# Optimization experiments

Measured on AMD Instinct MI355X. Metric: run time of the kernel, lower is better.

## Reference

```python
import jax, jax.numpy as jnp
import numpy as np

N_HEADS = 16
N_KV_HEADS = 4
HEAD_DIM = 128
D_MODEL = 2048
WINDOW = 1024
THETA = 10000.0
EPS = 1e-6


def _rmsnorm(x, w):
    var = jnp.mean(x * x, axis=-1, keepdims=True)
    return x * jax.lax.rsqrt(var + EPS) * w


def _rope(x, pos):
    # x: [B, H, S, D]; rotate-half (llama-style) RoPE
    d2 = HEAD_DIM // 2
    inv_freq = 1.0 / (THETA ** (jnp.arange(0, HEAD_DIM, 2, dtype=jnp.float32) / HEAD_DIM))
    ang = pos[:, None].astype(jnp.float32) * inv_freq[None, :]  # [S, D/2]
    cos = jnp.cos(ang)[None, None]
    sin = jnp.sin(ang)[None, None]
    x1, x2 = x[..., :d2], x[..., d2:]
    return jnp.concatenate([x1 * cos - x2 * sin, x1 * sin + x2 * cos], axis=-1)


def setup_inputs() -> dict:
    key = jax.random.key(0)
    ks = jax.random.split(key, 7)
    B, S = 1, 2048
    s = 0.02
    return {
        "x": jax.random.normal(ks[0], (B, S, D_MODEL), jnp.float32),
        "wq": jax.random.normal(ks[1], (N_HEADS * HEAD_DIM, D_MODEL), jnp.float32) * s,
        "wk": jax.random.normal(ks[2], (N_KV_HEADS * HEAD_DIM, D_MODEL), jnp.float32) * s,
        "wv": jax.random.normal(ks[3], (N_KV_HEADS * HEAD_DIM, D_MODEL), jnp.float32) * s,
        "wo": jax.random.normal(ks[4], (D_MODEL, N_HEADS * HEAD_DIM), jnp.float32) * s,
        "q_norm_w": jnp.ones((HEAD_DIM,), jnp.float32),
        "k_norm_w": jnp.ones((HEAD_DIM,), jnp.float32),
    }


def reference(x, wq, wk, wv, wo, q_norm_w, k_norm_w):
    B, S, _ = x.shape
    past_length = 0
    scale = HEAD_DIM ** -0.5
    n_rep = N_HEADS // N_KV_HEADS

    q = (x @ wq.T).reshape(B, S, N_HEADS, HEAD_DIM).transpose(0, 2, 1, 3)
    k = (x @ wk.T).reshape(B, S, N_KV_HEADS, HEAD_DIM).transpose(0, 2, 1, 3)
    v = (x @ wv.T).reshape(B, S, N_KV_HEADS, HEAD_DIM).transpose(0, 2, 1, 3)

    q = _rmsnorm(q, q_norm_w)
    k = _rmsnorm(k, k_norm_w)

    pos = jnp.arange(S) + past_length
    q = _rope(q, pos)
    k = _rope(k, pos)

    # GQA: materialize repeated KV heads, as in _repeat_kv
    k_rep = jnp.repeat(k, n_rep, axis=1)  # [B, H, S, D]
    v_rep = jnp.repeat(v, n_rep, axis=1)

    # sliding-window causal mask (total_seq_len=S > WINDOW)
    q_idx = jnp.arange(S)[:, None] + past_length
    k_idx = jnp.arange(S)[None, :]
    mask = (q_idx >= k_idx) & (q_idx - k_idx < WINDOW)  # [S, S]

    scores = jnp.einsum("bhqd,bhkd->bhqk", q, k_rep) * scale
    scores = jnp.where(mask[None, None], scores, jnp.float32(-jnp.inf))
    attn = jax.nn.softmax(scores, axis=-1)
    out = jnp.einsum("bhqk,bhkd->bhqd", attn, v_rep)

    out = out.transpose(0, 2, 1, 3).reshape(B, S, N_HEADS * HEAD_DIM)
    return out @ wo.T
```

## Files before the change

kernel.cpp:

```cpp
#include <hip/hip_runtime.h>
#include <hip/hip_bf16.h>
#include <cstdint>
#include <cstddef>

typedef __attribute__((ext_vector_type(4))) float f32x4;
typedef __attribute__((ext_vector_type(8))) short bf16x8;
typedef __attribute__((ext_vector_type(8))) unsigned short us8;

#define MFMA16(a, b, c) __builtin_amdgcn_mfma_f32_16x16x32_bf16(a, b, c, 0, 0, 0)

__device__ inline unsigned short f2bf(float f) {
    unsigned int u = __float_as_uint(f);
    u += 0x7fffu + ((u >> 16) & 1u);
    return (unsigned short)(u >> 16);
}
__device__ inline float bf2f(unsigned short u) {
    return __uint_as_float((unsigned int)u << 16);
}
__device__ inline unsigned short f2bf_fast(float f) {
    float r;
    asm("v_cvt_pk_bf16_f32 %0, %1, %2" : "=v"(r) : "v"(f), "v"(f));
    return (unsigned short)__float_as_uint(r);
}

__device__ inline void gload_lds16(const void* g, void* l) {
    __builtin_amdgcn_global_load_lds(
        (const __attribute__((address_space(1))) void*)g,
        (__attribute__((address_space(3))) void*)l, 16, 0, 0);
}
__device__ inline unsigned lds_addr(const void* p) {
    return (unsigned)(size_t)((__attribute__((address_space(3))) const void*)p);
}

__global__ __launch_bounds__(256) void prep_all(const float* __restrict__ x,
                                                const float* __restrict__ wq,
                                                const float* __restrict__ wk,
                                                const float* __restrict__ wv,
                                                const float* __restrict__ wo,
                                                unsigned short* __restrict__ xb,
                                                unsigned short* __restrict__ wqkv,
                                                unsigned short* __restrict__ wob,
                                                float2* __restrict__ tbl) {
    const int b = blockIdx.x;
    if (b < 14336) {
        const float* src; unsigned short* dst; int off4;
        if (b < 4096)       { src = x;  dst = xb;                 off4 = b; }
        else if (b < 8192)  { src = wq; dst = wqkv;               off4 = b - 4096; }
        else if (b < 9216)  { src = wk; dst = wqkv + 2048 * 2048; off4 = b - 8192; }
        else if (b < 10240) { src = wv; dst = wqkv + 2560 * 2048; off4 = b - 9216; }
        else                { src = wo; dst = wob;                off4 = b - 10240; }
        int i = (off4 * 256 + threadIdx.x) * 4;
        float4 v = *(const float4*)(src + i);
        ushort4 o;
        o.x = f2bf(v.x); o.y = f2bf(v.y); o.z = f2bf(v.z); o.w = f2bf(v.w);
        *(ushort4*)(dst + i) = o;
    } else {
        int idx = (b - 14336) * 256 + threadIdx.x;
        int row = idx >> 6, t = idx & 63;
        float inv_freq = exp2f((float)t * (-2.0f / 128.0f) * 13.287712379549449f);
        float s, c;
        sincosf((float)row * inv_freq, &s, &c);
        tbl[idx] = make_float2(c, s);
    }
}

__global__ __launch_bounds__(512, 2) void gemm256(const unsigned short* __restrict__ A,
                                                  const unsigned short* __restrict__ B,
                                                  unsigned short* __restrict__ Cp,
                                                  int M, int N, int Kfull, int kspan) {
    __shared__ unsigned short As[3][8192];
    __shared__ unsigned short Bs[3][8192];
    const int tid = threadIdx.x;
    const int lane = tid & 63, wave = tid >> 6;
    const int wr = wave >> 2, wc = wave & 3;
    const int l15 = lane & 15, l4 = lane >> 4;
    const int gx = gridDim.x;
    const int nwg = gx * gridDim.y;
    const int bid0 = blockIdx.y * gx + blockIdx.x;
    const int q8 = nwg >> 3, r8 = nwg & 7;
    const int xcd = bid0 & 7, sub = bid0 >> 3;
    const int wgid = ((xcd < r8) ? xcd * (q8 + 1) : r8 * (q8 + 1) + (xcd - r8) * q8) + sub;
    const int bm = wgid / gx, bn = wgid % gx;
    const int z = blockIdx.z;
    const unsigned short* Az = A + (size_t)z * kspan;
    const unsigned short* Bz = B + (size_t)z * kspan;
    unsigned short* C = Cp + (size_t)z * M * N;
    const int nK = kspan >> 5;

    f32x4 acc[8][4] = {};

    const int r0 = tid >> 2, qs = tid & 3;
    const int qsw = qs ^ ((r0 >> 1) & 3);
    const unsigned short* pa0 = Az + (size_t)(bm * 256 + r0) * Kfull + qsw * 8;
    const unsigned short* pa1 = pa0 + (size_t)128 * Kfull;
    const unsigned short* pb0 = Bz + (size_t)(bn * 256 + r0) * Kfull + qsw * 8;
    const unsigned short* pb1 = pb0 + (size_t)128 * Kfull;

#define STG(kt, bb)                                            \
    do {                                                       \
        gload_lds16(pa0 + (kt) * 32, &As[bb][tid * 8]);        \
        gload_lds16(pa1 + (kt) * 32, &As[bb][4096 + tid * 8]); \
        gload_lds16(pb0 + (kt) * 32, &Bs[bb][tid * 8]);        \
        gload_lds16(pb1 + (kt) * 32, &Bs[bb][4096 + tid * 8]); \
    } while (0)

    const int q = l4 ^ ((l15 >> 1) & 3);
    const unsigned aB = lds_addr(&As[0][0]) + (unsigned)((wr * 128 + l15) * 64 + q * 16);
    const unsigned bB = lds_addr(&Bs[0][0]) + (unsigned)((wc * 64 + l15) * 64 + q * 16);

#define DSR(dst, addr, off) \
    asm volatile("ds_read_b128 %0, %1 offset:" #off : "=v"(dst) : "v"(addr))

    STG(0, 0);
    STG(1, 1);
    int bc = 0, bs = 2;
    for (int kt = 0; kt < nK; ++kt) {
        if (kt + 1 < nK)
            asm volatile("s_waitcnt vmcnt(4)\ns_barrier" ::: "memory");
        else
            asm volatile("s_waitcnt vmcnt(0)\ns_barrier" ::: "memory");
        __builtin_amdgcn_sched_barrier(0);

        bf16x8 a[8], b[4];
        {
            const unsigned aA = aB + bc * 16384;
            const unsigned bA = bB + bc * 16384;
            DSR(b[0], bA, 0);    DSR(b[1], bA, 1024);
            DSR(b[2], bA, 2048); DSR(b[3], bA, 3072);
            DSR(a[0], aA, 0);    DSR(a[1], aA, 1024);
            DSR(a[2], aA, 2048); DSR(a[3], aA, 3072);
            DSR(a[4], aA, 4096); DSR(a[5], aA, 5120);
            DSR(a[6], aA, 6144); DSR(a[7], aA, 7168);
        }
        if (kt + 2 < nK) STG(kt + 2, bs);

        asm volatile("s_waitcnt lgkmcnt(4)" ::: "memory");
        __builtin_amdgcn_sched_barrier(0);
        __builtin_amdgcn_s_setprio(1);
#pragma unroll
        for (int m = 0; m < 4; ++m)
#pragma unroll
            for (int n = 0; n < 4; ++n)
                acc[m][n] = MFMA16(a[m], b[n], acc[m][n]);

        asm volatile("s_waitcnt lgkmcnt(0)" ::: "memory");
        __builtin_amdgcn_sched_barrier(0);
#pragma unroll
        for (int m = 4; m < 8; ++m)
#pragma unroll
            for (int n = 0; n < 4; ++n)
                acc[m][n] = MFMA16(a[m], b[n], acc[m][n]);
        __builtin_amdgcn_s_setprio(0);

        if (++bc == 3) bc = 0;
        if (++bs == 3) bs = 0;
    }
#undef STG
#undef DSR

    for (int m = 0; m < 8; ++m)
        for (int n = 0; n < 4; ++n)
            for (int j = 0; j < 4; ++j) {
                int row = bm * 256 + wr * 128 + m * 16 + l4 * 4 + j;
                int col = bn * 256 + wc * 64 + n * 16 + l15;
                C[(size_t)row * N + col] = f2bf_fast(acc[m][n][j]);
            }
}

__global__ __launch_bounds__(256) void norm_rope(const unsigned short* __restrict__ p0,
                                                 const unsigned short* __restrict__ p1,
                                                 const float* __restrict__ qw,
                                                 const float* __restrict__ kw,
                                                 const float2* __restrict__ tbl,
                                                 unsigned short* __restrict__ Qb,
                                                 unsigned short* __restrict__ Kb) {
    const int row = blockIdx.x;
    const int head = blockIdx.y * 4 + (threadIdx.x >> 6);
    const int t = threadIdx.x & 63;
    const size_t off = (size_t)row * 3072 + head * 128;
    float x1 = bf2f(p0[off + t]) + bf2f(p1[off + t]);
    float x2 = bf2f(p0[off + t + 64]) + bf2f(p1[off + t + 64]);
    float ss = x1 * x1 + x2 * x2;
    for (int m = 32; m; m >>= 1) ss += __shfl_xor(ss, m);
    float r = rsqrtf(ss * (1.0f / 128.0f) + 1e-6f);
    const float* w = (head < 16) ? qw : kw;
    float y1 = x1 * r * w[t], y2 = x2 * r * w[t + 64];
    float2 cs = tbl[row * 64 + t];
    x1 = y1 * cs.x - y2 * cs.y;
    x2 = y1 * cs.y + y2 * cs.x;
    if (head < 16) {
        const float SCALE2 = 0.12751879526654698f;
        x1 *= SCALE2; x2 *= SCALE2;
    }
    unsigned short* dst = (head < 16) ? Qb + ((size_t)head * 2048 + row) * 128
                                      : Kb + ((size_t)(head - 16) * 2048 + row) * 128;
    dst[t] = f2bf(x1);
    dst[t + 64] = f2bf(x2);
}

__global__ __launch_bounds__(256) void transpose_v(const unsigned short* __restrict__ p0,
                                                   const unsigned short* __restrict__ p1,
                                                   unsigned short* __restrict__ VbT) {
    const int kt = blockIdx.x;
    const int h  = blockIdx.y;
    __shared__ unsigned short T[64 * 132];
    const int tid = threadIdx.x;
    for (int i = 0; i < 8; ++i) {
        int s = i * 256 + tid;
        int r = s >> 5, c = (s & 31) * 4;
        size_t off = (size_t)(kt * 64 + r) * 3072 + (20 + h) * 128 + c;
        ushort4 a = *(const ushort4*)(p0 + off);
        ushort4 b = *(const ushort4*)(p1 + off);
        ushort4 o;
        o.x = f2bf(bf2f(a.x) + bf2f(b.x));
        o.y = f2bf(bf2f(a.y) + bf2f(b.y));
        o.z = f2bf(bf2f(a.z) + bf2f(b.z));
        o.w = f2bf(bf2f(a.w) + bf2f(b.w));
        *(ushort4*)&T[r * 132 + c] = o;
    }
    __syncthreads();
    for (int i = 0; i < 4; ++i) {
        int s = i * 256 + tid;
        int d = s >> 3, ck = (s & 7) * 8;
        us8 v;
        for (int j = 0; j < 8; ++j) {
            int c = ck + j;
            int k = (c & 3) * 16 + (c >> 2);
            v[j] = T[k * 132 + d];
        }
        *(us8*)(VbT + (size_t)h * 128 * 2048 + (size_t)d * 2048 + kt * 64 + ck) = v;
    }
}

__global__ __launch_bounds__(512) void attn_fwd(const unsigned short* __restrict__ Qb,
                                                const unsigned short* __restrict__ Kb,
                                                const unsigned short* __restrict__ VbT,
                                                unsigned short* __restrict__ Ob) {
    const int bid = blockIdx.x;
    const int p = bid & 7;
    const int qt = bid >> 3;
    const int q0 = qt * 64;
    __shared__ unsigned short Ks[2][64 * 128];
    __shared__ unsigned short Vs[128 * 64];
    __shared__ char PsB[8][16 * 136];
    const int tid = threadIdx.x;
    const int lane = tid & 63, wave = tid >> 6;
    const int l15 = lane & 15, l4 = lane >> 4;
    const int h = 2 * p + (wave >> 2);
    const int rgrp = wave & 3;
    const int kvh = p >> 1;

    bf16x8 qf[4];
    {
        const unsigned short* qrow =
            Qb + ((size_t)h * 2048 + q0 + rgrp * 16 + l15) * 128 + l4 * 8;
        for (int kk = 0; kk < 4; ++kk) qf[kk] = *(const bf16x8*)(qrow + kk * 32);
    }
    f32x4 o[8] = {};
    float m2[4], lp[4];
    for (int j = 0; j < 4; ++j) { m2[j] = -1e30f; lp[j] = 0.0f; }
    const int kt_lo = (qt >= 16) ? (qt - 16) : 0;

    const unsigned short* Kh = Kb + (size_t)kvh * 2048 * 128;
    const unsigned short* Vh = VbT + (size_t)kvh * 128 * 2048;

    int ksr[2], ksc[2], vsr[2], vsc[2];
    for (int i = 0; i < 2; ++i) {
        int s = i * 512 + tid;
        ksr[i] = s >> 4;
        ksc[i] = (((s & 15) * 16) ^ ((ksr[i] & 7) << 4)) >> 1;
        vsr[i] = s >> 3;
        vsc[i] = (((s & 7) * 16) ^ ((vsr[i] & 7) << 4)) >> 1;
    }

    for (int i = 0; i < 2; ++i)
        gload_lds16(Kh + (size_t)(kt_lo * 64 + ksr[i]) * 128 + ksc[i],
                    &Ks[0][(i * 512 + tid) * 8]);

    int cur = 0;
    for (int kt = kt_lo; kt <= qt; ++kt) {
        asm volatile("s_waitcnt vmcnt(0)\ns_barrier" ::: "memory");
        __builtin_amdgcn_sched_barrier(0);

        for (int i = 0; i < 2; ++i)
            gload_lds16(Vh + (size_t)vsr[i] * 2048 + kt * 64 + vsc[i],
                        &Vs[(i * 512 + tid) * 8]);
        if (kt < qt) {
            for (int i = 0; i < 2; ++i)
                gload_lds16(Kh + (size_t)((kt + 1) * 64 + ksr[i]) * 128 + ksc[i],
                            &Ks[cur ^ 1][(i * 512 + tid) * 8]);
        }

        f32x4 s[4] = {};
        __builtin_amdgcn_s_setprio(1);
        for (int nn = 0; nn < 4; ++nn)
            for (int kk = 0; kk < 4; ++kk) {
                int r = nn * 16 + l15;
                int cb = (kk * 64 + l4 * 16) ^ ((r & 7) << 4);
                bf16x8 kf = *(const bf16x8*)((const char*)&Ks[cur][0] + r * 256 + cb);
                s[nn] = MFMA16(qf[kk], kf, s[nn]);
            }
        __builtin_amdgcn_s_setprio(0);

        float pv4[4][4];
        const bool masked = (kt == qt) || (qt >= 16 && kt == kt_lo);
        if (masked) {
            for (int nn = 0; nn < 4; ++nn) {
                int kc = kt * 64 + nn * 16 + l15;
                for (int j = 0; j < 4; ++j) {
                    int qr = q0 + rgrp * 16 + l4 * 4 + j;
                    unsigned diff = (unsigned)(qr - kc);
                    pv4[nn][j] = (diff < 1024u) ? s[nn][j] : -1e30f;
                }
            }
        } else {
            for (int nn = 0; nn < 4; ++nn)
                for (int j = 0; j < 4; ++j) pv4[nn][j] = s[nn][j];
        }

        float mxl[4];
        bool flag = true;
        for (int j = 0; j < 4; ++j) {
            mxl[j] = fmaxf(fmaxf(pv4[0][j], pv4[1][j]), fmaxf(pv4[2][j], pv4[3][j]));
            flag = flag && (mxl[j] <= m2[j] + 11.0f);
        }
        if (!__all(flag)) {
            for (int j = 0; j < 4; ++j) {
                float mx = mxl[j];
                for (int mk = 8; mk; mk >>= 1) mx = fmaxf(mx, __shfl_xor(mx, mk));
                float mnew = fmaxf(m2[j], mx);
                float corr = exp2f(m2[j] - mnew);
                m2[j] = mnew;
                lp[j] *= corr;
                for (int dd = 0; dd < 8; ++dd) o[dd][j] *= corr;
            }
        }
        for (int j = 0; j < 4; ++j) {
            float rs = 0.0f;
            for (int nn = 0; nn < 4; ++nn) {
                float pv = exp2f(pv4[nn][j] - m2[j]);
                pv4[nn][j] = pv;
                rs += pv;
            }
            lp[j] += rs;
        }

        for (int j = 0; j < 4; ++j) {
            int row = l4 * 4 + j;
            unsigned lo, hi;
            asm("v_cvt_pk_bf16_f32 %0, %1, %2" : "=v"(lo) : "v"(pv4[0][j]), "v"(pv4[1][j]));
            asm("v_cvt_pk_bf16_f32 %0, %1, %2" : "=v"(hi) : "v"(pv4[2][j]), "v"(pv4[3][j]));
            int cb = (l15 * 8) ^ ((row & 7) << 4);
            *(uint2*)(&PsB[wave][0] + row * 136 + cb) = make_uint2(lo, hi);
        }

        bf16x8 pa[2];
        for (int kk2 = 0; kk2 < 2; ++kk2) {
            int cb = (kk2 * 64 + l4 * 16) ^ ((l15 & 7) << 4);
            pa[kk2] = *(const bf16x8*)(&PsB[wave][0] + l15 * 136 + cb);
        }

        if (kt < qt)
            asm volatile("s_waitcnt vmcnt(2)\ns_barrier" ::: "memory");
        else
            asm volatile("s_waitcnt vmcnt(0)\ns_barrier" ::: "memory");
        __builtin_amdgcn_sched_barrier(0);

        __builtin_amdgcn_s_setprio(1);
        for (int dd = 0; dd < 8; ++dd)
            for (int kk2 = 0; kk2 < 2; ++kk2) {
                int d = dd * 16 + l15;
                int cb = (kk2 * 64 + l4 * 16) ^ ((d & 7) << 4);
                bf16x8 vf = *(const bf16x8*)((const char*)&Vs[0] + d * 128 + cb);
                o[dd] = MFMA16(pa[kk2], vf, o[dd]);
            }
        __builtin_amdgcn_s_setprio(0);
        cur ^= 1;
    }

    for (int j = 0; j < 4; ++j) {
        float lt = lp[j];
        for (int mk = 8; mk; mk >>= 1) lt += __shfl_xor(lt, mk);
        float inv = 1.0f / lt;
        int row = q0 + rgrp * 16 + l4 * 4 + j;
        unsigned short* orow = Ob + (size_t)row * 2048 + h * 128;
        for (int dd = 0; dd < 8; ++dd) orow[dd * 16 + l15] = f2bf_fast(o[dd][j] * inv);
    }
}

__global__ __launch_bounds__(256) void add4(const unsigned short* __restrict__ p,
                                            float* __restrict__ out, int n) {
    int i = (blockIdx.x * 256 + threadIdx.x) * 8;
    if (i >= n) return;
    us8 a = *(const us8*)(p + i);
    us8 b = *(const us8*)(p + 4194304 + i);
    us8 c = *(const us8*)(p + 8388608 + i);
    us8 d = *(const us8*)(p + 12582912 + i);
    f32x4 o0, o1;
    for (int j = 0; j < 4; ++j)
        o0[j] = (bf2f(a[j]) + bf2f(b[j])) + (bf2f(c[j]) + bf2f(d[j]));
    for (int j = 0; j < 4; ++j)
        o1[j] = (bf2f(a[j + 4]) + bf2f(b[j + 4])) + (bf2f(c[j + 4]) + bf2f(d[j + 4]));
    *(f32x4*)(out + i) = o0;
    *(f32x4*)(out + i + 4) = o1;
}

extern "C" void kernel_launch(void* const* d_in, const int* in_sizes, int n_in,
                              void* d_out, int out_size, void* d_ws, size_t ws_size,
                              hipStream_t stream) {
    const float* x  = (const float*)d_in[0];
    const float* wq = (const float*)d_in[1];
    const float* wk = (const float*)d_in[2];
    const float* wv = (const float*)d_in[3];
    const float* wo = (const float*)d_in[4];
    const float* qw = (const float*)d_in[5];
    const float* kw = (const float*)d_in[6];
    float* out = (float*)d_out;

    char* ws = (char*)d_ws;
    unsigned short* xb   = (unsigned short*)(ws + 0);
    unsigned short* wqkv = (unsigned short*)(ws + 8388608);
    unsigned short* wob  = (unsigned short*)(ws + 20971520);
    unsigned short* qkvP = (unsigned short*)(ws + 29360128);
    unsigned short* Qb   = (unsigned short*)(ws + 54525952);
    unsigned short* Kb   = (unsigned short*)(ws + 62914560);
    unsigned short* VbT  = (unsigned short*)(ws + 65011712);
    unsigned short* Ob   = (unsigned short*)(ws + 67108864);
    unsigned short* outP = (unsigned short*)(ws + 29360128);
    float2*         tbl  = (float2*)(ws + 104857600);

    prep_all<<<dim3(14848), dim3(256), 0, stream>>>(x, wq, wk, wv, wo, xb, wqkv, wob, tbl);
    gemm256<<<dim3(12, 8, 2), dim3(512), 0, stream>>>(xb, wqkv, qkvP, 2048, 3072, 2048, 1024);
    norm_rope<<<dim3(2048, 5), dim3(256), 0, stream>>>(qkvP, qkvP + 2048 * 3072, qw, kw, tbl, Qb, Kb);
    transpose_v<<<dim3(32, 4), dim3(256), 0, stream>>>(qkvP, qkvP + 2048 * 3072, VbT);
    attn_fwd<<<dim3(256), dim3(512), 0, stream>>>(Qb, Kb, VbT, Ob);
    gemm256<<<dim3(8, 8, 4), dim3(512), 0, stream>>>(Ob, wob, outP, 2048, 2048, 2048, 512);
    add4<<<dim3(2048), dim3(256), 0, stream>>>(outP, out, 2048 * 2048);
}
```

Baseline: 127.1 us.

## Double the GEMM K-tile to 64 with double-buffered LDS and interleaved reads

Restructures the 256x256 GEMM mainloop. It now uses a K-step of 64 with two LDS buffers in place of three buffers of K=32, and a new XOR swizzle for 128-byte rows. LDS reads for the second K half are interleaved between MFMA groups, which halves the barrier count per K and overlaps LDS latency with compute. This costs occupancy: launch bounds drop to 1 block per CU because LDS use grows to 128KB. Only one stage of global prefetch remains, with a full vmcnt(0) wait each iteration.

After: 123.6 us. 1.03x faster.

```diff
diff --git a/kernel.cpp b/kernel.cpp
--- a/kernel.cpp
+++ b/kernel.cpp
@@ -64,12 +64,12 @@
     }
 }
 
-__global__ __launch_bounds__(512, 2) void gemm256(const unsigned short* __restrict__ A,
+__global__ __launch_bounds__(512, 1) void gemm256(const unsigned short* __restrict__ A,
                                                   const unsigned short* __restrict__ B,
                                                   unsigned short* __restrict__ Cp,
                                                   int M, int N, int Kfull, int kspan) {
-    __shared__ unsigned short As[3][8192];
-    __shared__ unsigned short Bs[3][8192];
+    __shared__ unsigned short As[2][256 * 64];
+    __shared__ unsigned short Bs[2][256 * 64];
     const int tid = threadIdx.x;
     const int lane = tid & 63, wave = tid >> 6;
     const int wr = wave >> 2, wc = wave & 3;
@@ -85,75 +85,123 @@
     const unsigned short* Az = A + (size_t)z * kspan;
     const unsigned short* Bz = B + (size_t)z * kspan;
     unsigned short* C = Cp + (size_t)z * M * N;
-    const int nK = kspan >> 5;
+    const int nK = kspan >> 6;
 
     f32x4 acc[8][4] = {};
 
-    const int r0 = tid >> 2, qs = tid & 3;
-    const int qsw = qs ^ ((r0 >> 1) & 3);
-    const unsigned short* pa0 = Az + (size_t)(bm * 256 + r0) * Kfull + qsw * 8;
-    const unsigned short* pa1 = pa0 + (size_t)128 * Kfull;
-    const unsigned short* pb0 = Bz + (size_t)(bn * 256 + r0) * Kfull + qsw * 8;
-    const unsigned short* pb1 = pb0 + (size_t)128 * Kfull;
-
-#define STG(kt, bb)                                            \
-    do {                                                       \
-        gload_lds16(pa0 + (kt) * 32, &As[bb][tid * 8]);        \
-        gload_lds16(pa1 + (kt) * 32, &As[bb][4096 + tid * 8]); \
-        gload_lds16(pb0 + (kt) * 32, &Bs[bb][tid * 8]);        \
-        gload_lds16(pb1 + (kt) * 32, &Bs[bb][4096 + tid * 8]); \
+    const int sA0 = tid, sA1 = 512 + tid, sA2 = 1024 + tid, sA3 = 1536 + tid;
+#define SRCOF(s) ((((((s) & 7) * 16) ^ ((((s) >> 3) & 7) << 4)) >> 1))
+    const unsigned short* pa0 = Az + (size_t)(bm * 256 + (sA0 >> 3)) * Kfull + SRCOF(sA0);
+    const unsigned short* pa1 = Az + (size_t)(bm * 256 + (sA1 >> 3)) * Kfull + SRCOF(sA1);
+    const unsigned short* pa2 = Az + (size_t)(bm * 256 + (sA2 >> 3)) * Kfull + SRCOF(sA2);
+    const unsigned short* pa3 = Az + (size_t)(bm * 256 + (sA3 >> 3)) * Kfull + SRCOF(sA3);
+    const unsigned short* pb0 = Bz + (size_t)(bn * 256 + (sA0 >> 3)) * Kfull + SRCOF(sA0);
+    const unsigned short* pb1 = Bz + (size_t)(bn * 256 + (sA1 >> 3)) * Kfull + SRCOF(sA1);
+    const unsigned short* pb2 = Bz + (size_t)(bn * 256 + (sA2 >> 3)) * Kfull + SRCOF(sA2);
+    const unsigned short* pb3 = Bz + (size_t)(bn * 256 + (sA3 >> 3)) * Kfull + SRCOF(sA3);
+#undef SRCOF
+
+#define STG(kt, bb)                                           \
+    do {                                                      \
+        gload_lds16(pa0 + (kt) * 64, &As[bb][sA0 * 8]);       \
+        gload_lds16(pa1 + (kt) * 64, &As[bb][sA1 * 8]);       \
+        gload_lds16(pa2 + (kt) * 64, &As[bb][sA2 * 8]);       \
+        gload_lds16(pa3 + (kt) * 64, &As[bb][sA3 * 8]);       \
+        gload_lds16(pb0 + (kt) * 64, &Bs[bb][sA0 * 8]);       \
+        gload_lds16(pb1 + (kt) * 64, &Bs[bb][sA1 * 8]);       \
+        gload_lds16(pb2 + (kt) * 64, &Bs[bb][sA2 * 8]);       \
+        gload_lds16(pb3 + (kt) * 64, &Bs[bb][sA3 * 8]);       \
     } while (0)
 
-    const int q = l4 ^ ((l15 >> 1) & 3);
-    const unsigned aB = lds_addr(&As[0][0]) + (unsigned)((wr * 128 + l15) * 64 + q * 16);
-    const unsigned bB = lds_addr(&Bs[0][0]) + (unsigned)((wc * 64 + l15) * 64 + q * 16);
+    const unsigned swz = (unsigned)((l4 * 16) ^ ((l15 & 7) << 4));
+    const unsigned aB0 = lds_addr(&As[0][0]) + (unsigned)((wr * 128 + l15) * 128) + swz;
+    const unsigned aB1 = aB0 ^ 64u;
+    const unsigned bB0 = lds_addr(&Bs[0][0]) + (unsigned)((wc * 64 + l15) * 128) + swz;
+    const unsigned bB1 = bB0 ^ 64u;
 
 #define DSR(dst, addr, off) \
     asm volatile("ds_read_b128 %0, %1 offset:" #off : "=v"(dst) : "v"(addr))
 
     STG(0, 0);
-    STG(1, 1);
-    int bc = 0, bs = 2;
     for (int kt = 0; kt < nK; ++kt) {
-        if (kt + 1 < nK)
-            asm volatile("s_waitcnt vmcnt(4)\ns_barrier" ::: "memory");
-        else
-            asm volatile("s_waitcnt vmcnt(0)\ns_barrier" ::: "memory");
-        __builtin_amdgcn_sched_barrier(0);
-
-        bf16x8 a[8], b[4];
-        {
-            const unsigned aA = aB + bc * 16384;
-            const unsigned bA = bB + bc * 16384;
-            DSR(b[0], bA, 0);    DSR(b[1], bA, 1024);
-            DSR(b[2], bA, 2048); DSR(b[3], bA, 3072);
-            DSR(a[0], aA, 0);    DSR(a[1], aA, 1024);
-            DSR(a[2], aA, 2048); DSR(a[3], aA, 3072);
-            DSR(a[4], aA, 4096); DSR(a[5], aA, 5120);
-            DSR(a[6], aA, 6144); DSR(a[7], aA, 7168);
-        }
-        if (kt + 2 < nK) STG(kt + 2, bs);
+        const int bc = kt & 1;
+        asm volatile("s_waitcnt vmcnt(0)\ns_barrier" ::: "memory");
+        __builtin_amdgcn_sched_barrier(0);
+
+        const unsigned aA0 = aB0 + bc * 32768, aA1 = aB1 + bc * 32768;
+        const unsigned bA0 = bB0 + bc * 32768, bA1 = bB1 + bc * 32768;
+        bf16x8 a00, a01, a02, a03, a04, a05, a06, a07;
+        bf16x8 a10, a11, a12, a13, a14, a15, a16, a17;
+        bf16x8 b00, b01, b02, b03, b10, b11, b12, b13;
+
+        DSR(b00, bA0, 0);    DSR(b01, bA0, 2048);
+        DSR(b02, bA0, 4096); DSR(b03, bA0, 6144);
+        DSR(a00, aA0, 0);    DSR(a01, aA0, 2048);
+        DSR(a02, aA0, 4096); DSR(a03, aA0, 6144);
+        DSR(a04, aA0, 8192);  DSR(a05, aA0, 10240);
+        DSR(a06, aA0, 12288); DSR(a07, aA0, 14336);
+
+        if (kt + 1 < nK) STG(kt + 1, bc ^ 1);
 
         asm volatile("s_waitcnt lgkmcnt(4)" ::: "memory");
         __builtin_amdgcn_sched_barrier(0);
         __builtin_amdgcn_s_setprio(1);
-#pragma unroll
-        for (int m = 0; m < 4; ++m)
-#pragma unroll
-            for (int n = 0; n < 4; ++n)
-                acc[m][n] = MFMA16(a[m], b[n], acc[m][n]);
+        acc[0][0] = MFMA16(a00, b00, acc[0][0]); acc[0][1] = MFMA16(a00, b01, acc[0][1]);
+        acc[0][2] = MFMA16(a00, b02, acc[0][2]); acc[0][3] = MFMA16(a00, b03, acc[0][3]);
+        acc[1][0] = MFMA16(a01, b00, acc[1][0]); acc[1][1] = MFMA16(a01, b01, acc[1][1]);
+        acc[1][2] = MFMA16(a01, b02, acc[1][2]); acc[1][3] = MFMA16(a01, b03, acc[1][3]);
+        acc[2][0] = MFMA16(a02, b00, acc[2][0]); acc[2][1] = MFMA16(a02, b01, acc[2][1]);
+        acc[2][2] = MFMA16(a02, b02, acc[2][2]); acc[2][3] = MFMA16(a02, b03, acc[2][3]);
+        acc[3][0] = MFMA16(a03, b00, acc[3][0]); acc[3][1] = MFMA16(a03, b01, acc[3][1]);
+        acc[3][2] = MFMA16(a03, b02, acc[3][2]); acc[3][3] = MFMA16(a03, b03, acc[3][3]);
+        __builtin_amdgcn_s_setprio(0);
+
+        DSR(b10, bA1, 0);    DSR(b11, bA1, 2048);
+        DSR(b12, bA1, 4096); DSR(b13, bA1, 6144);
+        DSR(a10, aA1, 0);    DSR(a11, aA1, 2048);
+        DSR(a12, aA1, 4096); DSR(a13, aA1, 6144);
+
+        asm volatile("s_waitcnt lgkmcnt(8)" ::: "memory");
+        __builtin_amdgcn_sched_barrier(0);
+        __builtin_amdgcn_s_setprio(1);
+        acc[4][0] = MFMA16(a04, b00, acc[4][0]); acc[4][1] = MFMA16(a04, b01, acc[4][1]);
+        acc[4][2] = MFMA16(a04, b02, acc[4][2]); acc[4][3] = MFMA16(a04, b03, acc[4][3]);
+        acc[5][0] = MFMA16(a05, b00, acc[5][0]); acc[5][1] = MFMA16(a05, b01, acc[5][1]);
+        acc[5][2] = MFMA16(a05, b02, acc[5][2]); acc[5][3] = MFMA16(a05, b03, acc[5][3]);
+        acc[6][0] = MFMA16(a06, b00, acc[6][0]); acc[6][1] = MFMA16(a06, b01, acc[6][1]);
+        acc[6][2] = MFMA16(a06, b02, acc[6][2]); acc[6][3] = MFMA16(a06, b03, acc[6][3]);
+        acc[7][0] = MFMA16(a07, b00, acc[7][0]); acc[7][1] = MFMA16(a07, b01, acc[7][1]);
+        acc[7][2] = MFMA16(a07, b02, acc[7][2]); acc[7][3] = MFMA16(a07, b03, acc[7][3]);
+        __builtin_amdgcn_s_setprio(0);
+
+        DSR(a14, aA1, 8192);  DSR(a15, aA1, 10240);
+        DSR(a16, aA1, 12288); DSR(a17, aA1, 14336);
+
+        asm volatile("s_waitcnt lgkmcnt(4)" ::: "memory");
+        __builtin_amdgcn_sched_barrier(0);
+        __builtin_amdgcn_s_setprio(1);
+        acc[0][0] = MFMA16(a10, b10, acc[0][0]); acc[0][1] = MFMA16(a10, b11, acc[0][1]);
+        acc[0][2] = MFMA16(a10, b12, acc[0][2]); acc[0][3] = MFMA16(a10, b13, acc[0][3]);
+        acc[1][0] = MFMA16(a11, b10, acc[1][0]); acc[1][1] = MFMA16(a11, b11, acc[1][1]);
+        acc[1][2] = MFMA16(a11, b12, acc[1][2]); acc[1][3] = MFMA16(a11, b13, acc[1][3]);
+        acc[2][0] = MFMA16(a12, b10, acc[2][0]); acc[2][1] = MFMA16(a12, b11, acc[2][1]);
+        acc[2][2] = MFMA16(a12, b12, acc[2][2]); acc[2][3] = MFMA16(a12, b13, acc[2][3]);
+        acc[3][0] = MFMA16(a13, b10, acc[3][0]); acc[3][1] = MFMA16(a13, b11, acc[3][1]);
+        acc[3][2] = MFMA16(a13, b12, acc[3][2]); acc[3][3] = MFMA16(a13, b13, acc[3][3]);
+        __builtin_amdgcn_s_setprio(0);
 
         asm volatile("s_waitcnt lgkmcnt(0)" ::: "memory");
         __builtin_amdgcn_sched_barrier(0);
-#pragma unroll
-        for (int m = 4; m < 8; ++m)
-#pragma unroll
-            for (int n = 0; n < 4; ++n)
-                acc[m][n] = MFMA16(a[m], b[n], acc[m][n]);
-        __builtin_amdgcn_s_setprio(0);
-
-        if (++bc == 3) bc = 0;
-        if (++bs == 3) bs = 0;
+        __builtin_amdgcn_s_setprio(1);
+        acc[4][0] = MFMA16(a14, b10, acc[4][0]); acc[4][1] = MFMA16(a14, b11, acc[4][1]);
+        acc[4][2] = MFMA16(a14, b12, acc[4][2]); acc[4][3] = MFMA16(a14, b13, acc[4][3]);
+        acc[5][0] = MFMA16(a15, b10, acc[5][0]); acc[5][1] = MFMA16(a15, b11, acc[5][1]);
+        acc[5][2] = MFMA16(a15, b12, acc[5][2]); acc[5][3] = MFMA16(a15, b13, acc[5][3]);
+        acc[6][0] = MFMA16(a16, b10, acc[6][0]); acc[6][1] = MFMA16(a16, b11, acc[6][1]);
+        acc[6][2] = MFMA16(a16, b12, acc[6][2]); acc[6][3] = MFMA16(a16, b13, acc[6][3]);
+        acc[7][0] = MFMA16(a17, b10, acc[7][0]); acc[7][1] = MFMA16(a17, b11, acc[7][1]);
+        acc[7][2] = MFMA16(a17, b12, acc[7][2]); acc[7][3] = MFMA16(a17, b13, acc[7][3]);
+        __builtin_amdgcn_s_setprio(0);
     }
 #undef STG
 #undef DSR
```
